# Kernel tuning notes

Hardware: AMD Instinct MI355X
Metric: run time of the kernel (lower is better)

The kernel has to match this reference:

```python
import jax, jax.numpy as jnp
import numpy as np

B, L, R, E, H = 256, 196, 1024, 1024, 512  # batch, regions, rnn_size, input_encoding, att_hid


def _lstm_cell(x, h, c, Wih, Whh, bih, bhh):
    # PyTorch LSTMCell gate order: i, f, g, o
    gates = x @ Wih.T + bih + h @ Whh.T + bhh  # [B, 4R]
    i, f, g, o = jnp.split(gates, 4, axis=1)
    i, f, o = jax.nn.sigmoid(i), jax.nn.sigmoid(f), jax.nn.sigmoid(o)
    g = jnp.tanh(g)
    c_new = f * c + i * g
    h_new = o * jnp.tanh(c_new)
    return h_new, c_new


def _attention(h, att_feats, p_att, mask, Wh, bh, Wa, ba):
    att_h = h @ Wh.T + bh                       # [B, H]
    dot = jnp.tanh(p_att + att_h[:, None, :])   # [B, L, H]
    scores = jnp.einsum('blh,h->bl', dot, Wa) + ba  # [B, L]
    w = jax.nn.softmax(scores, axis=1)
    w = w * mask
    w = w / (jnp.sum(w, axis=1, keepdims=True) + 1e-10)
    return jnp.einsum('bl,bld->bd', w, att_feats)  # [B, R]


def setup_inputs() -> dict:
    key = jax.random.key(0)
    ks = jax.random.split(key, 32)
    s = 0.05
    inp = {
        'xt': jax.random.normal(ks[0], (B, E), jnp.float32),
        'fc_feats': jax.random.normal(ks[1], (B, 3 * R), jnp.float32),
        'att_feats': jax.random.normal(ks[2], (B, L, R), jnp.float32),
        'p_att_feats': jax.random.normal(ks[3], (B, L, H), jnp.float32),
        'att_masks': jnp.ones((B, L), jnp.float32),
        'att_feats1': jax.random.normal(ks[4], (B, L, R), jnp.float32),
        'p_att_feats1': jax.random.normal(ks[5], (B, L, H), jnp.float32),
        'att_masks1': jnp.ones((B, L), jnp.float32),
        'state_h': jax.random.normal(ks[6], (3, B, R), jnp.float32),
        'state_c': jax.random.normal(ks[7], (3, B, R), jnp.float32),
        # att_lstm0 / att_lstm: input dim E + 2R; lang_lstm: 3R
        'Wih0': jax.random.normal(ks[8], (4 * R, E + 2 * R), jnp.float32) * s,
        'Whh0': jax.random.normal(ks[9], (4 * R, R), jnp.float32) * s,
        'bih0': jnp.zeros((4 * R,), jnp.float32),
        'bhh0': jnp.zeros((4 * R,), jnp.float32),
        'Wih1': jax.random.normal(ks[10], (4 * R, E + 2 * R), jnp.float32) * s,
        'Whh1': jax.random.normal(ks[11], (4 * R, R), jnp.float32) * s,
        'bih1': jnp.zeros((4 * R,), jnp.float32),
        'bhh1': jnp.zeros((4 * R,), jnp.float32),
        'WihL': jax.random.normal(ks[12], (4 * R, 3 * R), jnp.float32) * s,
        'WhhL': jax.random.normal(ks[13], (4 * R, R), jnp.float32) * s,
        'bihL': jnp.zeros((4 * R,), jnp.float32),
        'bhhL': jnp.zeros((4 * R,), jnp.float32),
        # attention0 / attention / attention1 params (h2att + alpha_net)
        'a0_Wh': jax.random.normal(ks[14], (H, R), jnp.float32) * s,
        'a0_bh': jnp.zeros((H,), jnp.float32),
        'a0_Wa': jax.random.normal(ks[15], (H,), jnp.float32) * s,
        'a0_ba': jnp.zeros((), jnp.float32),
        'a_Wh': jax.random.normal(ks[16], (H, R), jnp.float32) * s,
        'a_bh': jnp.zeros((H,), jnp.float32),
        'a_Wa': jax.random.normal(ks[17], (H,), jnp.float32) * s,
        'a_ba': jnp.zeros((), jnp.float32),
        'a1_Wh': jax.random.normal(ks[18], (H, R), jnp.float32) * s,
        'a1_bh': jnp.zeros((H,), jnp.float32),
        'a1_Wa': jax.random.normal(ks[19], (H,), jnp.float32) * s,
        'a1_ba': jnp.zeros((), jnp.float32),
    }
    return inp


def reference(xt, fc_feats, att_feats, p_att_feats, att_masks,
              att_feats1, p_att_feats1, att_masks1, state_h, state_c,
              Wih0, Whh0, bih0, bhh0, Wih1, Whh1, bih1, bhh1,
              WihL, WhhL, bihL, bhhL,
              a0_Wh, a0_bh, a0_Wa, a0_ba,
              a_Wh, a_bh, a_Wa, a_ba,
              a1_Wh, a1_bh, a1_Wa, a1_ba):
    prev_h = state_h[-1]                       # h_lang from previous step
    fc_ori = fc_feats[:, :R]                   # only the first slice is used

    # layer 0: att_lstm0 + attention0 over (att_feats1, p_att_feats1)
    x0 = jnp.concatenate([prev_h, fc_ori, xt], axis=1)
    h_att0, c_att0 = _lstm_cell(x0, state_h[0], state_c[0], Wih0, Whh0, bih0, bhh0)
    att0 = _attention(h_att0, att_feats1, p_att_feats1, att_masks1, a0_Wh, a0_bh, a0_Wa, a0_ba)

    # layer 1: att_lstm + two attentions
    x1 = jnp.concatenate([prev_h, att0, xt], axis=1)
    h_att, c_att = _lstm_cell(x1, state_h[1], state_c[1], Wih1, Whh1, bih1, bhh1)
    att = _attention(h_att, att_feats, p_att_feats, att_masks, a_Wh, a_bh, a_Wa, a_ba)
    att1 = _attention(h_att, att_feats1, p_att_feats1, att_masks1, a1_Wh, a1_bh, a1_Wa, a1_ba)

    # layer 2: lang_lstm
    xL = jnp.concatenate([att, att1, h_att], axis=1)
    h_lang, c_lang = _lstm_cell(xL, state_h[2], state_c[2], WihL, WhhL, bihL, bhhL)

    output = h_lang  # dropout is identity in eval mode
    new_h = jnp.stack([h_att0, h_att, h_lang])
    new_c = jnp.stack([c_att0, c_att, c_lang])
    return output, new_h, new_c
```

## Files before the change

kernel.cpp:

```cpp
#include <hip/hip_runtime.h>
#include <math.h>

#define B_   256
#define L_   196
#define R_   1024
#define E_   1024
#define H_   512
#define G4R  4096
#define DIN  3072

typedef short v4s __attribute__((ext_vector_type(4)));
typedef short v8s __attribute__((ext_vector_type(8)));
typedef float v4f __attribute__((ext_vector_type(4)));

__device__ __forceinline__ float sigmoidf_(float x) {
    return 1.0f / (1.0f + __expf(-x));
}
__device__ __forceinline__ float tanhf_(float x) {
    float ax = fabsf(x);
    float t  = __expf(-2.0f * ax);
    float r  = (1.0f - t) / (1.0f + t);
    return copysignf(r, x);
}

__device__ __forceinline__ void split2(float x, short& hi, short& lo) {
    unsigned u = __float_as_uint(x);
    hi = (short)(u >> 16);
    float r = x - __uint_as_float(u & 0xFFFF0000u);
    lo = (short)(__float_as_uint(r) >> 16);
}

template<int MT, int NT>
__global__ __launch_bounds__(256) void gemm_mfma(
    const float* __restrict__ A1, const float* __restrict__ W1, int K1, int lda1,
    const float* __restrict__ A2, const float* __restrict__ W2, int K2, int lda2,
    const float* __restrict__ bias1, const float* __restrict__ bias2,
    float* __restrict__ C, int N)
{
    constexpr int FM  = MT / 32;
    constexpr int FN  = NT / 32;
    constexpr int ACH = (MT * 32) / 1024;
    constexpr int WCH = (NT * 32) / 1024;

    __shared__ alignas(16) short Ahi[MT][40];
    __shared__ alignas(16) short Alo[MT][40];
    __shared__ alignas(16) short Whi[NT][40];
    __shared__ alignas(16) short Wlo[NT][40];

    const int t     = threadIdx.x;
    const int lane  = t & 63;
    const int wave  = t >> 6;
    const int waveM = wave & 1;
    const int waveN = wave >> 1;
    const int l16   = lane & 15;
    const int quad  = lane >> 4;
    const int mBase = blockIdx.x * MT;
    const int nBase = blockIdx.y * NT;

    v4f acc[FM][FN] = {};

    for (int seg = 0; seg < 2; ++seg) {
        const int K = seg ? K2 : K1;
        if (K == 0) continue;
        const float* Ag  = seg ? A2 : A1;
        const float* Wg  = seg ? W2 : W1;
        const int    lda = seg ? lda2 : lda1;

        for (int k0 = 0; k0 < K; k0 += 32) {
            __syncthreads();
            #pragma unroll
            for (int c = 0; c < ACH; ++c) {
                int flat = t * 4 + c * 1024;
                int row  = flat >> 5, k = flat & 31;
                float4 v = *(const float4*)(Ag + (size_t)(mBase + row) * lda + k0 + k);
                short h0, h1, h2, h3, l0, l1, l2, l3;
                split2(v.x, h0, l0); split2(v.y, h1, l1);
                split2(v.z, h2, l2); split2(v.w, h3, l3);
                v4s hv = { h0, h1, h2, h3 };
                v4s lv = { l0, l1, l2, l3 };
                *(v4s*)&Ahi[row][k] = hv;
                *(v4s*)&Alo[row][k] = lv;
            }
            #pragma unroll
            for (int c = 0; c < WCH; ++c) {
                int flat = t * 4 + c * 1024;
                int row  = flat >> 5, k = flat & 31;
                float4 v = *(const float4*)(Wg + (size_t)(nBase + row) * K + k0 + k);
                short h0, h1, h2, h3, l0, l1, l2, l3;
                split2(v.x, h0, l0); split2(v.y, h1, l1);
                split2(v.z, h2, l2); split2(v.w, h3, l3);
                v4s hv = { h0, h1, h2, h3 };
                v4s lv = { l0, l1, l2, l3 };
                *(v4s*)&Whi[row][k] = hv;
                *(v4s*)&Wlo[row][k] = lv;
            }
            __syncthreads();

            v8s ah[FM], al[FM], wh[FN], wl[FN];
            #pragma unroll
            for (int fi = 0; fi < FM; ++fi) {
                int r = waveM * (MT / 2) + fi * 16 + l16;
                ah[fi] = *(const v8s*)&Ahi[r][quad * 8];
                al[fi] = *(const v8s*)&Alo[r][quad * 8];
            }
            #pragma unroll
            for (int fj = 0; fj < FN; ++fj) {
                int r = waveN * (NT / 2) + fj * 16 + l16;
                wh[fj] = *(const v8s*)&Whi[r][quad * 8];
                wl[fj] = *(const v8s*)&Wlo[r][quad * 8];
            }

            #pragma unroll
            for (int fi = 0; fi < FM; ++fi)
                #pragma unroll
                for (int fj = 0; fj < FN; ++fj) {
                    acc[fi][fj] = __builtin_amdgcn_mfma_f32_16x16x32_bf16(
                        al[fi], wh[fj], acc[fi][fj], 0, 0, 0);
                    acc[fi][fj] = __builtin_amdgcn_mfma_f32_16x16x32_bf16(
                        ah[fi], wl[fj], acc[fi][fj], 0, 0, 0);
                    acc[fi][fj] = __builtin_amdgcn_mfma_f32_16x16x32_bf16(
                        ah[fi], wh[fj], acc[fi][fj], 0, 0, 0);
                }
        }
    }

    #pragma unroll
    for (int fj = 0; fj < FN; ++fj) {
        int n = nBase + waveN * (NT / 2) + fj * 16 + l16;
        float bb = bias1[n] + (bias2 ? bias2[n] : 0.0f);
        #pragma unroll
        for (int fi = 0; fi < FM; ++fi) {
            int m0 = mBase + waveM * (MT / 2) + fi * 16 + quad * 4;
            #pragma unroll
            for (int r = 0; r < 4; ++r)
                C[(size_t)(m0 + r) * N + n] = acc[fi][fj][r] + bb;
        }
    }
}

__global__ __launch_bounds__(256) void lstm_cell(
    const float* __restrict__ gates, const float* __restrict__ c_in,
    float* __restrict__ h_out, float* __restrict__ c_out,
    float* __restrict__ h_out2)
{
    int e = blockIdx.x * 256 + threadIdx.x;
    int b = e >> 10;
    int j = e & 1023;
    const float* g = gates + (size_t)b * G4R;
    float i_ = sigmoidf_(g[j]);
    float f_ = sigmoidf_(g[j + 1024]);
    float gg = tanhf_(g[j + 2048]);
    float o_ = sigmoidf_(g[j + 3072]);
    float c  = f_ * c_in[e] + i_ * gg;
    float h  = o_ * tanhf_(c);
    c_out[e] = c;
    h_out[e] = h;
    if (h_out2) h_out2[e] = h;
}

__global__ __launch_bounds__(256) void concat3_1024(
    float* __restrict__ dst,
    const float* __restrict__ s0, int ld0,
    const float* __restrict__ s1, int ld1,
    const float* __restrict__ s2, int ld2)
{
    int e = blockIdx.x * 256 + threadIdx.x;
    int b = e / 3072;
    int c = e - b * 3072;
    int which = c >> 10, off = c & 1023;
    const float* s = (which == 0) ? s0 : (which == 1) ? s1 : s2;
    int ld = (which == 0) ? ld0 : (which == 1) ? ld1 : ld2;
    dst[e] = s[(size_t)b * ld + off];
}

__global__ __launch_bounds__(64) void attn_scores(
    const float* __restrict__ p_att,
    const float* __restrict__ att_h,
    const float* __restrict__ Wa,
    const float* __restrict__ ba,
    float* __restrict__ scores)
{
    int l = blockIdx.x;
    int b = blockIdx.y;
    int lane = threadIdx.x;
    const float* p  = p_att + ((size_t)b * L_ + l) * H_;
    const float* ah = att_h + (size_t)b * H_;
    float sum = 0.0f;
#pragma unroll
    for (int i = 0; i < H_ / 64; i++) {
        int h = lane + i * 64;
        sum += tanhf_(p[h] + ah[h]) * Wa[h];
    }
    for (int off = 32; off; off >>= 1) sum += __shfl_down(sum, off);
    if (lane == 0) scores[(size_t)b * L_ + l] = sum + ba[0];
}

__global__ __launch_bounds__(256) void attn_softmax(
    const float* __restrict__ scores, const float* __restrict__ mask,
    float* __restrict__ w)
{
    int b = blockIdx.x;
    int t = threadIdx.x;
    __shared__ float red[256];
    float v = (t < L_) ? scores[(size_t)b * L_ + t] : -1e30f;
    red[t] = v; __syncthreads();
    for (int s = 128; s; s >>= 1) {
        if (t < s) red[t] = fmaxf(red[t], red[t + s]);
        __syncthreads();
    }
    float mx = red[0]; __syncthreads();
    float e = (t < L_) ? __expf(v - mx) : 0.0f;
    red[t] = e; __syncthreads();
    for (int s = 128; s; s >>= 1) {
        if (t < s) red[t] += red[t + s];
        __syncthreads();
    }
    float denom = red[0]; __syncthreads();
    float wm = (t < L_) ? (e / denom) * mask[(size_t)b * L_ + t] : 0.0f;
    red[t] = wm; __syncthreads();
    for (int s = 128; s; s >>= 1) {
        if (t < s) red[t] += red[t + s];
        __syncthreads();
    }
    float denom2 = red[0] + 1e-10f;
    if (t < L_) w[(size_t)b * L_ + t] = wm / denom2;
}

__global__ __launch_bounds__(256) void attn_wsum(
    const float* __restrict__ w,
    const float* __restrict__ feats,
    float* __restrict__ out)
{
    int b = blockIdx.y;
    int r = blockIdx.x * 256 + threadIdx.x;
    __shared__ float ws[L_];
    for (int i = threadIdx.x; i < L_; i += 256)
        ws[i] = w[(size_t)b * L_ + i];
    __syncthreads();
    const float* f = feats + (size_t)b * L_ * R_ + r;
    float a0 = 0, a1 = 0, a2 = 0, a3 = 0;
    for (int l = 0; l < L_; l += 4) {
        a0 += ws[l + 0] * f[(size_t)(l + 0) * R_];
        a1 += ws[l + 1] * f[(size_t)(l + 1) * R_];
        a2 += ws[l + 2] * f[(size_t)(l + 2) * R_];
        a3 += ws[l + 3] * f[(size_t)(l + 3) * R_];
    }
    out[(size_t)b * R_ + r] = a0 + a1 + a2 + a3;
}

extern "C" void kernel_launch(void* const* d_in, const int* in_sizes, int n_in,
                              void* d_out, int out_size, void* d_ws, size_t ws_size,
                              hipStream_t stream)
{
    const float* xt         = (const float*)d_in[0];
    const float* fc_feats   = (const float*)d_in[1];
    const float* att_feats  = (const float*)d_in[2];
    const float* p_att      = (const float*)d_in[3];
    const float* mask       = (const float*)d_in[4];
    const float* att_feats1 = (const float*)d_in[5];
    const float* p_att1     = (const float*)d_in[6];
    const float* mask1      = (const float*)d_in[7];
    const float* state_h    = (const float*)d_in[8];
    const float* state_c    = (const float*)d_in[9];
    const float* Wih0 = (const float*)d_in[10];
    const float* Whh0 = (const float*)d_in[11];
    const float* bih0 = (const float*)d_in[12];
    const float* bhh0 = (const float*)d_in[13];
    const float* Wih1 = (const float*)d_in[14];
    const float* Whh1 = (const float*)d_in[15];
    const float* bih1 = (const float*)d_in[16];
    const float* bhh1 = (const float*)d_in[17];
    const float* WihL = (const float*)d_in[18];
    const float* WhhL = (const float*)d_in[19];
    const float* bihL = (const float*)d_in[20];
    const float* bhhL = (const float*)d_in[21];
    const float* a0_Wh = (const float*)d_in[22];
    const float* a0_bh = (const float*)d_in[23];
    const float* a0_Wa = (const float*)d_in[24];
    const float* a0_ba = (const float*)d_in[25];
    const float* a_Wh  = (const float*)d_in[26];
    const float* a_bh  = (const float*)d_in[27];
    const float* a_Wa  = (const float*)d_in[28];
    const float* a_ba  = (const float*)d_in[29];
    const float* a1_Wh = (const float*)d_in[30];
    const float* a1_bh = (const float*)d_in[31];
    const float* a1_Wa = (const float*)d_in[32];
    const float* a1_ba = (const float*)d_in[33];

    const size_t BR = (size_t)B_ * R_;
    float* out   = (float*)d_out;
    float* h0    = out + 1 * BR;
    float* h1    = out + 2 * BR;
    float* h2    = out + 3 * BR;
    float* c0    = out + 4 * BR;
    float* c1    = out + 5 * BR;
    float* c2    = out + 6 * BR;

    float* xbuf  = (float*)d_ws;
    float* gates = xbuf + (size_t)B_ * DIN;
    float* atth  = gates + (size_t)B_ * G4R;
    float* sc    = atth + (size_t)B_ * H_;
    float* att0  = sc + (size_t)B_ * L_;
    float* attA  = att0 + BR;
    float* attB  = attA + BR;

    const float* prev_h = state_h + 2 * BR;

    dim3 gG(B_ / 64, G4R / 64);
    dim3 gA(B_ / 32, H_ / 32);
    dim3 gS(L_, B_);
    dim3 gW(R_ / 256, B_);

    concat3_1024<<<(B_ * DIN) / 256, 256, 0, stream>>>(xbuf, prev_h, R_, fc_feats, 3 * R_, xt, E_);
    gemm_mfma<64, 64><<<gG, 256, 0, stream>>>(xbuf, Wih0, DIN, DIN,
                                              state_h, Whh0, R_, R_,
                                              bih0, bhh0, gates, G4R);
    lstm_cell<<<(B_ * R_) / 256, 256, 0, stream>>>(gates, state_c, h0, c0, nullptr);

    gemm_mfma<32, 32><<<gA, 256, 0, stream>>>(h0, a0_Wh, R_, R_,
                                              nullptr, nullptr, 0, 0,
                                              a0_bh, nullptr, atth, H_);
    attn_scores<<<gS, 64, 0, stream>>>(p_att1, atth, a0_Wa, a0_ba, sc);
    attn_softmax<<<B_, 256, 0, stream>>>(sc, mask1, sc);
    attn_wsum<<<gW, 256, 0, stream>>>(sc, att_feats1, att0);

    concat3_1024<<<(B_ * DIN) / 256, 256, 0, stream>>>(xbuf, prev_h, R_, att0, R_, xt, E_);
    gemm_mfma<64, 64><<<gG, 256, 0, stream>>>(xbuf, Wih1, DIN, DIN,
                                              state_h + BR, Whh1, R_, R_,
                                              bih1, bhh1, gates, G4R);
    lstm_cell<<<(B_ * R_) / 256, 256, 0, stream>>>(gates, state_c + BR, h1, c1, nullptr);

    gemm_mfma<32, 32><<<gA, 256, 0, stream>>>(h1, a_Wh, R_, R_,
                                              nullptr, nullptr, 0, 0,
                                              a_bh, nullptr, atth, H_);
    attn_scores<<<gS, 64, 0, stream>>>(p_att, atth, a_Wa, a_ba, sc);
    attn_softmax<<<B_, 256, 0, stream>>>(sc, mask, sc);
    attn_wsum<<<gW, 256, 0, stream>>>(sc, att_feats, attA);

    gemm_mfma<32, 32><<<gA, 256, 0, stream>>>(h1, a1_Wh, R_, R_,
                                              nullptr, nullptr, 0, 0,
                                              a1_bh, nullptr, atth, H_);
    attn_scores<<<gS, 64, 0, stream>>>(p_att1, atth, a1_Wa, a1_ba, sc);
    attn_softmax<<<B_, 256, 0, stream>>>(sc, mask1, sc);
    attn_wsum<<<gW, 256, 0, stream>>>(sc, att_feats1, attB);

    concat3_1024<<<(B_ * DIN) / 256, 256, 0, stream>>>(xbuf, attA, R_, attB, R_, h1, R_);
    gemm_mfma<64, 64><<<gG, 256, 0, stream>>>(xbuf, WihL, DIN, DIN,
                                              state_h + 2 * BR, WhhL, R_, R_,
                                              bihL, bhhL, gates, G4R);
    lstm_cell<<<(B_ * R_) / 256, 256, 0, stream>>>(gates, state_c + 2 * BR, h2, c2, out);
}
```

Before: 1.215 ms.

## Split-K GEMMs with register-prefetch double buffering, drop concat, vectorize attention kernels

Replaces the GEMM with a split-K version that reads the four input segments directly, so the concat kernels are no longer needed. It double-buffers LDS with register prefetch and remaps blocks in an XCD-aware order. Partial sums are reduced inside lstm_cell and a new att_hsum kernel. attn_scores packs four rows per block with float4 loads, and attn_wsum processes a whole batch row per block with float4 loads. This raises parallelism and hides load latency, at the cost of extra partial-sum traffic and a larger workspace.

```diff
diff --git a/kernel.cpp b/kernel.cpp
--- a/kernel.cpp
+++ b/kernel.cpp
@@ -30,22 +30,28 @@
     lo = (short)(__float_as_uint(r) >> 16);
 }
 
-template<int MT, int NT>
-__global__ __launch_bounds__(256) void gemm_mfma(
-    const float* __restrict__ A1, const float* __restrict__ W1, int K1, int lda1,
-    const float* __restrict__ A2, const float* __restrict__ W2, int K2, int lda2,
+__device__ __forceinline__ void fma4(float4& a, float s, const float4& v) {
+    a.x += s * v.x; a.y += s * v.y; a.z += s * v.z; a.w += s * v.w;
+}
+
+template<int MT>
+__global__ __launch_bounds__(256, 4) void gemm_sk(
+    const float* __restrict__ a0, int lda0,
+    const float* __restrict__ a1, int lda1,
+    const float* __restrict__ a2, int lda2,
+    const float* __restrict__ a3, int lda3,
+    const float* __restrict__ w0, int ldw0,
+    const float* __restrict__ w1, int ldw1,
+    const float* __restrict__ w2, int ldw2,
+    const float* __restrict__ w3, int ldw3,
     const float* __restrict__ bias1, const float* __restrict__ bias2,
-    float* __restrict__ C, int N)
-{
-    constexpr int FM  = MT / 32;
-    constexpr int FN  = NT / 32;
-    constexpr int ACH = (MT * 32) / 1024;
-    constexpr int WCH = (NT * 32) / 1024;
-
-    __shared__ alignas(16) short Ahi[MT][40];
-    __shared__ alignas(16) short Alo[MT][40];
-    __shared__ alignas(16) short Whi[NT][40];
-    __shared__ alignas(16) short Wlo[NT][40];
+    float* __restrict__ C, int N,
+    int lgM, int KSm1, int lgKS, int nt)
+{
+    constexpr int FM = MT / 32;
+    constexpr int CH = MT / 32;
+
+    __shared__ alignas(16) short lds[2][4][MT][40];
 
     const int t     = threadIdx.x;
     const int lane  = t & 63;
@@ -54,103 +60,137 @@
     const int waveN = wave >> 1;
     const int l16   = lane & 15;
     const int quad  = lane >> 4;
-    const int mBase = blockIdx.x * MT;
-    const int nBase = blockIdx.y * NT;
-
-    v4f acc[FM][FN] = {};
-
-    for (int seg = 0; seg < 2; ++seg) {
-        const int K = seg ? K2 : K1;
-        if (K == 0) continue;
-        const float* Ag  = seg ? A2 : A1;
-        const float* Wg  = seg ? W2 : W1;
-        const int    lda = seg ? lda2 : lda1;
-
-        for (int k0 = 0; k0 < K; k0 += 32) {
-            __syncthreads();
-            #pragma unroll
-            for (int c = 0; c < ACH; ++c) {
-                int flat = t * 4 + c * 1024;
-                int row  = flat >> 5, k = flat & 31;
-                float4 v = *(const float4*)(Ag + (size_t)(mBase + row) * lda + k0 + k);
-                short h0, h1, h2, h3, l0, l1, l2, l3;
-                split2(v.x, h0, l0); split2(v.y, h1, l1);
-                split2(v.z, h2, l2); split2(v.w, h3, l3);
-                v4s hv = { h0, h1, h2, h3 };
-                v4s lv = { l0, l1, l2, l3 };
-                *(v4s*)&Ahi[row][k] = hv;
-                *(v4s*)&Alo[row][k] = lv;
+
+    const int bid = blockIdx.x;
+    const int wg  = (bid & 7) * (gridDim.x >> 3) + (bid >> 3);
+    const int m    = wg & ((1 << lgM) - 1);
+    const int rest = wg >> lgM;
+    const int kc   = rest & KSm1;
+    const int n    = rest >> lgKS;
+    const int mBase = m * MT;
+    const int nBase = n * MT;
+    const int t0    = kc * nt;
+
+    const int rowA = t >> 3;
+    const int kkA  = (t & 7) * 4;
+
+    v4f acc[FM][FM] = {};
+
+    auto loadT = [&](int i, float4* RA, float4* RW) {
+        const int s  = (i >> 5) & 3;
+        const int k0 = (i & 31) << 5;
+        const float* pa = (s == 0) ? a0 : (s == 1) ? a1 : (s == 2) ? a2 : a3;
+        const int    la = (s == 0) ? lda0 : (s == 1) ? lda1 : (s == 2) ? lda2 : lda3;
+        const float* pw = (s == 0) ? w0 : (s == 1) ? w1 : (s == 2) ? w2 : w3;
+        const int    lw = (s == 0) ? ldw0 : (s == 1) ? ldw1 : (s == 2) ? ldw2 : ldw3;
+        pa += (size_t)(mBase + rowA) * la + k0 + kkA;
+        pw += (size_t)(nBase + rowA) * lw + k0 + kkA;
+#pragma unroll
+        for (int c = 0; c < CH; ++c) {
+            RA[c] = *(const float4*)(pa + (size_t)(c * 32) * la);
+            RW[c] = *(const float4*)(pw + (size_t)(c * 32) * lw);
+        }
+    };
+
+    auto storeT = [&](int buf, const float4* RA, const float4* RW) {
+#pragma unroll
+        for (int c = 0; c < CH; ++c) {
+            const int row = rowA + c * 32;
+            short h0, h1, h2, h3, l0, l1, l2, l3;
+            split2(RA[c].x, h0, l0); split2(RA[c].y, h1, l1);
+            split2(RA[c].z, h2, l2); split2(RA[c].w, h3, l3);
+            v4s hv = { h0, h1, h2, h3 };
+            v4s lv = { l0, l1, l2, l3 };
+            *(v4s*)&lds[buf][0][row][kkA] = hv;
+            *(v4s*)&lds[buf][1][row][kkA] = lv;
+            split2(RW[c].x, h0, l0); split2(RW[c].y, h1, l1);
+            split2(RW[c].z, h2, l2); split2(RW[c].w, h3, l3);
+            v4s hw = { h0, h1, h2, h3 };
+            v4s lw = { l0, l1, l2, l3 };
+            *(v4s*)&lds[buf][2][row][kkA] = hw;
+            *(v4s*)&lds[buf][3][row][kkA] = lw;
+        }
+    };
+
+    auto compT = [&](int buf) {
+        v8s ah[FM], al[FM], wh[FM], wl[FM];
+#pragma unroll
+        for (int fi = 0; fi < FM; ++fi) {
+            int r = waveM * (MT / 2) + fi * 16 + l16;
+            ah[fi] = *(const v8s*)&lds[buf][0][r][quad * 8];
+            al[fi] = *(const v8s*)&lds[buf][1][r][quad * 8];
+        }
+#pragma unroll
+        for (int fj = 0; fj < FM; ++fj) {
+            int r = waveN * (MT / 2) + fj * 16 + l16;
+            wh[fj] = *(const v8s*)&lds[buf][2][r][quad * 8];
+            wl[fj] = *(const v8s*)&lds[buf][3][r][quad * 8];
+        }
+#pragma unroll
+        for (int fi = 0; fi < FM; ++fi)
+#pragma unroll
+            for (int fj = 0; fj < FM; ++fj) {
+                acc[fi][fj] = __builtin_amdgcn_mfma_f32_16x16x32_bf16(
+                    al[fi], wh[fj], acc[fi][fj], 0, 0, 0);
+                acc[fi][fj] = __builtin_amdgcn_mfma_f32_16x16x32_bf16(
+                    ah[fi], wl[fj], acc[fi][fj], 0, 0, 0);
+                acc[fi][fj] = __builtin_amdgcn_mfma_f32_16x16x32_bf16(
+                    ah[fi], wh[fj], acc[fi][fj], 0, 0, 0);
             }
-            #pragma unroll
-            for (int c = 0; c < WCH; ++c) {
-                int flat = t * 4 + c * 1024;
-                int row  = flat >> 5, k = flat & 31;
-                float4 v = *(const float4*)(Wg + (size_t)(nBase + row) * K + k0 + k);
-                short h0, h1, h2, h3, l0, l1, l2, l3;
-                split2(v.x, h0, l0); split2(v.y, h1, l1);
-                split2(v.z, h2, l2); split2(v.w, h3, l3);
-                v4s hv = { h0, h1, h2, h3 };
-                v4s lv = { l0, l1, l2, l3 };
-                *(v4s*)&Whi[row][k] = hv;
-                *(v4s*)&Wlo[row][k] = lv;
-            }
-            __syncthreads();
-
-            v8s ah[FM], al[FM], wh[FN], wl[FN];
-            #pragma unroll
-            for (int fi = 0; fi < FM; ++fi) {
-                int r = waveM * (MT / 2) + fi * 16 + l16;
-                ah[fi] = *(const v8s*)&Ahi[r][quad * 8];
-                al[fi] = *(const v8s*)&Alo[r][quad * 8];
-            }
-            #pragma unroll
-            for (int fj = 0; fj < FN; ++fj) {
-                int r = waveN * (NT / 2) + fj * 16 + l16;
-                wh[fj] = *(const v8s*)&Whi[r][quad * 8];
-                wl[fj] = *(const v8s*)&Wlo[r][quad * 8];
-            }
-
-            #pragma unroll
-            for (int fi = 0; fi < FM; ++fi)
-                #pragma unroll
-                for (int fj = 0; fj < FN; ++fj) {
-                    acc[fi][fj] = __builtin_amdgcn_mfma_f32_16x16x32_bf16(
-                        al[fi], wh[fj], acc[fi][fj], 0, 0, 0);
-                    acc[fi][fj] = __builtin_amdgcn_mfma_f32_16x16x32_bf16(
-                        ah[fi], wl[fj], acc[fi][fj], 0, 0, 0);
-                    acc[fi][fj] = __builtin_amdgcn_mfma_f32_16x16x32_bf16(
-                        ah[fi], wh[fj], acc[fi][fj], 0, 0, 0);
-                }
-        }
-    }
-
-    #pragma unroll
-    for (int fj = 0; fj < FN; ++fj) {
-        int n = nBase + waveN * (NT / 2) + fj * 16 + l16;
-        float bb = bias1[n] + (bias2 ? bias2[n] : 0.0f);
-        #pragma unroll
+    };
+
+    float4 rA0[CH], rW0[CH], rA1[CH], rW1[CH];
+    loadT(t0, rA0, rW0);
+
+#pragma unroll 1
+    for (int i = 0; i < nt; i += 2) {
+        storeT(0, rA0, rW0);
+        loadT(t0 + i + 1, rA1, rW1);
+        __syncthreads();
+        compT(0);
+        storeT(1, rA1, rW1);
+        if (i + 2 < nt) loadT(t0 + i + 2, rA0, rW0);
+        __syncthreads();
+        compT(1);
+    }
+
+    float* Cp = C + (size_t)kc * B_ * N;
+#pragma unroll
+    for (int fj = 0; fj < FM; ++fj) {
+        int nn = nBase + waveN * (MT / 2) + fj * 16 + l16;
+        float bb = 0.0f;
+        if (kc == 0 && bias1) bb = bias1[nn] + (bias2 ? bias2[nn] : 0.0f);
+#pragma unroll
         for (int fi = 0; fi < FM; ++fi) {
             int m0 = mBase + waveM * (MT / 2) + fi * 16 + quad * 4;
-            #pragma unroll
+#pragma unroll
             for (int r = 0; r < 4; ++r)
-                C[(size_t)(m0 + r) * N + n] = acc[fi][fj][r] + bb;
+                Cp[(size_t)(m0 + r) * N + nn] = acc[fi][fj][r] + bb;
         }
     }
 }
 
 __global__ __launch_bounds__(256) void lstm_cell(
-    const float* __restrict__ gates, const float* __restrict__ c_in,
+    const float* __restrict__ gp, int nparts,
+    const float* __restrict__ c_in,
     float* __restrict__ h_out, float* __restrict__ c_out,
     float* __restrict__ h_out2)
 {
     int e = blockIdx.x * 256 + threadIdx.x;
     int b = e >> 10;
     int j = e & 1023;
-    const float* g = gates + (size_t)b * G4R;
-    float i_ = sigmoidf_(g[j]);
-    float f_ = sigmoidf_(g[j + 1024]);
-    float gg = tanhf_(g[j + 2048]);
-    float o_ = sigmoidf_(g[j + 3072]);
+    float s0 = 0, s1 = 0, s2 = 0, s3 = 0;
+    for (int p = 0; p < nparts; ++p) {
+        const float* g = gp + (size_t)p * B_ * G4R + (size_t)b * G4R;
+        s0 += g[j];
+        s1 += g[j + 1024];
+        s2 += g[j + 2048];
+        s3 += g[j + 3072];
+    }
+    float i_ = sigmoidf_(s0);
+    float f_ = sigmoidf_(s1);
+    float gg = tanhf_(s2);
+    float o_ = sigmoidf_(s3);
     float c  = f_ * c_in[e] + i_ * gg;
     float h  = o_ * tanhf_(c);
     c_out[e] = c;
@@ -158,41 +198,42 @@
     if (h_out2) h_out2[e] = h;
 }
 
-__global__ __launch_bounds__(256) void concat3_1024(
-    float* __restrict__ dst,
-    const float* __restrict__ s0, int ld0,
-    const float* __restrict__ s1, int ld1,
-    const float* __restrict__ s2, int ld2)
+__global__ __launch_bounds__(256) void att_hsum(
+    const float* __restrict__ parts, int nparts,
+    const float* __restrict__ bh, float* __restrict__ atth)
 {
     int e = blockIdx.x * 256 + threadIdx.x;
-    int b = e / 3072;
-    int c = e - b * 3072;
-    int which = c >> 10, off = c & 1023;
-    const float* s = (which == 0) ? s0 : (which == 1) ? s1 : s2;
-    int ld = (which == 0) ? ld0 : (which == 1) ? ld1 : ld2;
-    dst[e] = s[(size_t)b * ld + off];
-}
-
-__global__ __launch_bounds__(64) void attn_scores(
+    float s = bh[e & (H_ - 1)];
+    for (int p = 0; p < nparts; ++p)
+        s += parts[(size_t)p * B_ * H_ + e];
+    atth[e] = s;
+}
+
+__global__ __launch_bounds__(256) void attn_scores(
     const float* __restrict__ p_att,
     const float* __restrict__ att_h,
     const float* __restrict__ Wa,
     const float* __restrict__ ba,
     float* __restrict__ scores)
 {
-    int l = blockIdx.x;
+    int w    = threadIdx.x >> 6;
+    int lane = threadIdx.x & 63;
+    int l = blockIdx.x * 4 + w;
     int b = blockIdx.y;
-    int lane = threadIdx.x;
-    const float* p  = p_att + ((size_t)b * L_ + l) * H_;
-    const float* ah = att_h + (size_t)b * H_;
-    float sum = 0.0f;
-#pragma unroll
-    for (int i = 0; i < H_ / 64; i++) {
-        int h = lane + i * 64;
-        sum += tanhf_(p[h] + ah[h]) * Wa[h];
-    }
-    for (int off = 32; off; off >>= 1) sum += __shfl_down(sum, off);
-    if (lane == 0) scores[(size_t)b * L_ + l] = sum + ba[0];
+    const float4* p   = (const float4*)(p_att + ((size_t)b * L_ + l) * H_);
+    const float4* ah  = (const float4*)(att_h + (size_t)b * H_);
+    const float4* wa4 = (const float4*)Wa;
+    float s = 0.0f;
+#pragma unroll
+    for (int i = 0; i < H_ / 256; i++) {
+        float4 pv = p[lane + i * 64];
+        float4 av = ah[lane + i * 64];
+        float4 wv = wa4[lane + i * 64];
+        s += tanhf_(pv.x + av.x) * wv.x + tanhf_(pv.y + av.y) * wv.y
+           + tanhf_(pv.z + av.z) * wv.z + tanhf_(pv.w + av.w) * wv.w;
+    }
+    for (int off = 32; off; off >>= 1) s += __shfl_down(s, off);
+    if (lane == 0) scores[(size_t)b * L_ + l] = s + ba[0];
 }
 
 __global__ __launch_bounds__(256) void attn_softmax(
@@ -231,21 +272,29 @@
     const float* __restrict__ feats,
     float* __restrict__ out)
 {
-    int b = blockIdx.y;
-    int r = blockIdx.x * 256 + threadIdx.x;
+    int b = blockIdx.x;
+    int t = threadIdx.x;
     __shared__ float ws[L_];
-    for (int i = threadIdx.x; i < L_; i += 256)
-        ws[i] = w[(size_t)b * L_ + i];
+    if (t < L_) ws[t] = w[(size_t)b * L_ + t];
     __syncthreads();
-    const float* f = feats + (size_t)b * L_ * R_ + r;
-    float a0 = 0, a1 = 0, a2 = 0, a3 = 0;
+    const float4* f = (const float4*)(feats + (size_t)b * L_ * R_) + t;
+    float4 a0 = {0,0,0,0}, a1 = {0,0,0,0}, a2 = {0,0,0,0}, a3 = {0,0,0,0};
     for (int l = 0; l < L_; l += 4) {
-        a0 += ws[l + 0] * f[(size_t)(l + 0) * R_];
-        a1 += ws[l + 1] * f[(size_t)(l + 1) * R_];
-        a2 += ws[l + 2] * f[(size_t)(l + 2) * R_];
-        a3 += ws[l + 3] * f[(size_t)(l + 3) * R_];
-    }
-    out[(size_t)b * R_ + r] = a0 + a1 + a2 + a3;
+        float4 v0 = f[(size_t)(l + 0) * 256];
+        float4 v1 = f[(size_t)(l + 1) * 256];
+        float4 v2 = f[(size_t)(l + 2) * 256];
+        float4 v3 = f[(size_t)(l + 3) * 256];
+        fma4(a0, ws[l + 0], v0);
+        fma4(a1, ws[l + 1], v1);
+        fma4(a2, ws[l + 2], v2);
+        fma4(a3, ws[l + 3], v3);
+    }
+    float4 r;
+    r.x = a0.x + a1.x + a2.x + a3.x;
+    r.y = a0.y + a1.y + a2.y + a3.y;
+    r.z = a0.z + a1.z + a2.z + a3.z;
+    r.w = a0.w + a1.w + a2.w + a3.w;
+    ((float4*)(out + (size_t)b * R_))[t] = r;
 }
 
 extern "C" void kernel_launch(void* const* d_in, const int* in_sizes, int n_in,
@@ -296,57 +345,73 @@
     float* c1    = out + 5 * BR;
     float* c2    = out + 6 * BR;
 
-    float* xbuf  = (float*)d_ws;
-    float* gates = xbuf + (size_t)B_ * DIN;
-    float* atth  = gates + (size_t)B_ * G4R;
-    float* sc    = atth + (size_t)B_ * H_;
-    float* att0  = sc + (size_t)B_ * L_;
-    float* attA  = att0 + BR;
-    float* attB  = attA + BR;
+    int KSB = 4, KSA = 4;
+    {
+        size_t need = ((size_t)KSB * B_ * G4R + (size_t)KSA * B_ * H_ +
+                       (size_t)B_ * H_ + (size_t)B_ * L_ + 3 * BR) * sizeof(float);
+        if (ws_size < need) { KSB = 1; KSA = 1; }
+    }
+    const int lgKSB = (KSB == 4) ? 2 : 0;
+    const int lgKSA = (KSA == 4) ? 2 : 0;
+    const int ntB = 128 / KSB;
+    const int ntA = 32 / KSA;
+
+    float* gatesp = (float*)d_ws;
+    float* atthp  = gatesp + (size_t)KSB * B_ * G4R;
+    float* atth   = atthp + (size_t)KSA * B_ * H_;
+    float* sc     = atth + (size_t)B_ * H_;
+    float* att0   = sc + (size_t)B_ * L_;
+    float* attA   = att0 + BR;
+    float* attB   = attA + BR;
 
     const float* prev_h = state_h + 2 * BR;
 
-    dim3 gG(B_ / 64, G4R / 64);
-    dim3 gA(B_ / 32, H_ / 32);
-    dim3 gS(L_, B_);
-    dim3 gW(R_ / 256, B_);
-
-    concat3_1024<<<(B_ * DIN) / 256, 256, 0, stream>>>(xbuf, prev_h, R_, fc_feats, 3 * R_, xt, E_);
-    gemm_mfma<64, 64><<<gG, 256, 0, stream>>>(xbuf, Wih0, DIN, DIN,
-                                              state_h, Whh0, R_, R_,
-                                              bih0, bhh0, gates, G4R);
-    lstm_cell<<<(B_ * R_) / 256, 256, 0, stream>>>(gates, state_c, h0, c0, nullptr);
-
-    gemm_mfma<32, 32><<<gA, 256, 0, stream>>>(h0, a0_Wh, R_, R_,
-                                              nullptr, nullptr, 0, 0,
-                                              a0_bh, nullptr, atth, H_);
-    attn_scores<<<gS, 64, 0, stream>>>(p_att1, atth, a0_Wa, a0_ba, sc);
+    dim3 gBig(256 * KSB);
+    dim3 gAtt(128 * KSA);
+    dim3 gS(49, B_);
+
+    gemm_sk<64><<<gBig, 256, 0, stream>>>(
+        prev_h, R_, fc_feats, 3 * R_, xt, E_, state_h, R_,
+        Wih0, DIN, Wih0 + 1024, DIN, Wih0 + 2048, DIN, Whh0, R_,
+        bih0, bhh0, gatesp, G4R, 2, KSB - 1, lgKSB, ntB);
+    lstm_cell<<<(B_ * R_) / 256, 256, 0, stream>>>(gatesp, KSB, state_c, h0, c0, nullptr);
+
+    gemm_sk<32><<<gAtt, 256, 0, stream>>>(
+        h0, R_, h0, R_, h0, R_, h0, R_,
+        a0_Wh, R_, a0_Wh, R_, a0_Wh, R_, a0_Wh, R_,
+        nullptr, nullptr, atthp, H_, 3, KSA - 1, lgKSA, ntA);
+    att_hsum<<<(B_ * H_) / 256, 256, 0, stream>>>(atthp, KSA, a0_bh, atth);
+    attn_scores<<<gS, 256, 0, stream>>>(p_att1, atth, a0_Wa, a0_ba, sc);
     attn_softmax<<<B_, 256, 0, stream>>>(sc, mask1, sc);
-    attn_wsum<<<gW, 256, 0, stream>>>(sc, att_feats1, att0);
-
-    concat3_1024<<<(B_ * DIN) / 256, 256, 0, stream>>>(xbuf, prev_h, R_, att0, R_, xt, E_);
-    gemm_mfma<64, 64><<<gG, 256, 0, stream>>>(xbuf, Wih1, DIN, DIN,
-                                              state_h + BR, Whh1, R_, R_,
-                                              bih1, bhh1, gates, G4R);
-    lstm_cell<<<(B_ * R_) / 256, 256, 0, stream>>>(gates, state_c + BR, h1, c1, nullptr);
-
-    gemm_mfma<32, 32><<<gA, 256, 0, stream>>>(h1, a_Wh, R_, R_,
-                                              nullptr, nullptr, 0, 0,
-                                              a_bh, nullptr, atth, H_);
-    attn_scores<<<gS, 64, 0, stream>>>(p_att, atth, a_Wa, a_ba, sc);
+    attn_wsum<<<B_, 256, 0, stream>>>(sc, att_feats1, att0);
+
+    gemm_sk<64><<<gBig, 256, 0, stream>>>(
+        prev_h, R_, att0, R_, xt, E_, state_h + BR, R_,
+        Wih1, DIN, Wih1 + 1024, DIN, Wih1 + 2048, DIN, Whh1, R_,
+        bih1, bhh1, gatesp, G4R, 2, KSB - 1, lgKSB, ntB);
+    lstm_cell<<<(B_ * R_) / 256, 256, 0, stream>>>(gatesp, KSB, state_c + BR, h1, c1, nullptr);
+
+    gemm_sk<32><<<gAtt, 256, 0, stream>>>(
+        h1, R_, h1, R_, h1, R_, h1, R_,
+        a_Wh, R_, a_Wh, R_, a_Wh, R_, a_Wh, R_,
+        nullptr, nullptr, atthp, H_, 3, KSA - 1, lgKSA, ntA);
+    att_hsum<<<(B_ * H_) / 256, 256, 0, stream>>>(atthp, KSA, a_bh, atth);
+    attn_scores<<<gS, 256, 0, stream>>>(p_att, atth, a_Wa, a_ba, sc);
     attn_softmax<<<B_, 256, 0, stream>>>(sc, mask, sc);
-    attn_wsum<<<gW, 256, 0, stream>>>(sc, att_feats, attA);
-
-    gemm_mfma<32, 32><<<gA, 256, 0, stream>>>(h1, a1_Wh, R_, R_,
-                                              nullptr, nullptr, 0, 0,
-                                              a1_bh, nullptr, atth, H_);
-    attn_scores<<<gS, 64, 0, stream>>>(p_att1, atth, a1_Wa, a1_ba, sc);
+    attn_wsum<<<B_, 256, 0, stream>>>(sc, att_feats, attA);
+
+    gemm_sk<32><<<gAtt, 256, 0, stream>>>(
+        h1, R_, h1, R_, h1, R_, h1, R_,
+        a1_Wh, R_, a1_Wh, R_, a1_Wh, R_, a1_Wh, R_,
+        nullptr, nullptr, atthp, H_, 3, KSA - 1, lgKSA, ntA);
+    att_hsum<<<(B_ * H_) / 256, 256, 0, stream>>>(atthp, KSA, a1_bh, atth);
+    attn_scores<<<gS, 256, 0, stream>>>(p_att1, atth, a1_Wa, a1_ba, sc);
     attn_softmax<<<B_, 256, 0, stream>>>(sc, mask1, sc);
-    attn_wsum<<<gW, 256, 0, stream>>>(sc, att_feats1, attB);
-
-    concat3_1024<<<(B_ * DIN) / 256, 256, 0, stream>>>(xbuf, attA, R_, attB, R_, h1, R_);
-    gemm_mfma<64, 64><<<gG, 256, 0, stream>>>(xbuf, WihL, DIN, DIN,
-                                              state_h + 2 * BR, WhhL, R_, R_,
-                                              bihL, bhhL, gates, G4R);
-    lstm_cell<<<(B_ * R_) / 256, 256, 0, stream>>>(gates, state_c + 2 * BR, h2, c2, out);
-}
+    attn_wsum<<<B_, 256, 0, stream>>>(sc, att_feats1, attB);
+
+    gemm_sk<64><<<gBig, 256, 0, stream>>>(
+        attA, R_, attB, R_, h1, R_, state_h + 2 * BR, R_,
+        WihL, DIN, WihL + 1024, DIN, WihL + 2048, DIN, WhhL, R_,
+        bihL, bhhL, gatesp, G4R, 2, KSB - 1, lgKSB, ntB);
+    lstm_cell<<<(B_ * R_) / 256, 256, 0, stream>>>(gatesp, KSB, state_c + 2 * BR, h2, c2, out);
+}
```

Result: faster. 1.171 ms (-3.6%).
